# Performance work log

Measured on AMD Instinct MI355X. Metric: run time of the kernel, lower is better.

## Reference

```python
import jax, jax.numpy as jnp
import numpy as np

B, C, L = 8, 512, 2048


def setup_inputs() -> dict:
    key = jax.random.key(0)
    ks = jax.random.split(key, 7)
    s = 1.0 / np.sqrt(C)
    return {
        "x": jax.random.normal(ks[0], (B, C, L), dtype=jnp.float32),
        "Wq": jax.random.normal(ks[1], (C, C), dtype=jnp.float32) * s,
        "bq": jax.random.normal(ks[2], (C,), dtype=jnp.float32) * s,
        "Wk": jax.random.normal(ks[3], (C, C), dtype=jnp.float32) * s,
        "bk": jax.random.normal(ks[4], (C,), dtype=jnp.float32) * s,
        "Wv": jax.random.normal(ks[5], (C, C), dtype=jnp.float32) * s,
        "bv": jax.random.normal(ks[6], (C,), dtype=jnp.float32) * s,
    }


def reference(x, Wq, bq, Wk, bk, Wv, bv):
    # Conv1d(kernel_size=1) == per-position linear: [C_out, C_in] @ x[b,:,l]
    q = jnp.einsum('oi,bil->bol', Wq, x) + bq[None, :, None]  # [B, C, L]
    k = jnp.einsum('oi,bil->bol', Wk, x) + bk[None, :, None]
    v = jnp.einsum('oi,bil->bol', Wv, x) + bv[None, :, None]
    scale = 1.0 / jnp.sqrt(jnp.asarray(x.shape[1], dtype=x.dtype))
    # scores[b, l, m] = sum_c q[b,c,l] * k[b,c,m] / sqrt(C)
    scores = jnp.einsum('bcl,bcm->blm', q, k) * scale  # [B, L, L]
    attn = jax.nn.softmax(scores, axis=-1)
    # out[b, c, l] = sum_m v[b,c,m] * attn[b,l,m]   (== bmm(V, attn^T))
    return jnp.einsum('bcm,blm->bcl', v, attn)  # [B, C, L]
```

## Files before the change

### kernel.cpp

```cpp
#include <hip/hip_runtime.h>
#include <hip/hip_bf16.h>
#include <math.h>

#define B 8
#define C 512
#define L 2048

using bf16x8 = __bf16 __attribute__((ext_vector_type(8)));
using f32x4  = float __attribute__((ext_vector_type(4)));

#define MFMA(a, b, c) __builtin_amdgcn_mfma_f32_16x16x32_bf16((a), (b), (c), 0, 0, 0)
#define SC2 0.06375872f
#define SH2 -17.312340f

__device__ __forceinline__ unsigned short f2bf(float f) {
    unsigned int u; __builtin_memcpy(&u, &f, 4);
    u += 0x7FFF + ((u >> 16) & 1);
    return (unsigned short)(u >> 16);
}
__device__ __forceinline__ void load_lds16(const unsigned short* g, unsigned short* l) {
    __builtin_amdgcn_global_load_lds(
        (const __attribute__((address_space(1))) unsigned int*)g,
        (__attribute__((address_space(3))) unsigned int*)l, 16, 0, 0);
}

template<int MODE, int KDIM>
__device__ __forceinline__ void gemm_core(
    const unsigned short* __restrict__ A,
    const unsigned short* __restrict__ Bm,
    unsigned short* As, unsigned short* Bs,
    void* __restrict__ OutV, int ldo,
    float* __restrict__ ep)
{
    const int t = threadIdx.x;
    const int wave = t >> 6, lane = t & 63;
    const int ll = t & 15, quad = (t >> 4) & 3;
    const int lr = lane >> 2, chunk = lane & 3;
    const int wm = (wave & 1) * 64, wn = (wave >> 1) * 64;

    const unsigned short* gA0 = A  + (size_t)(wave * 32 + lr) * KDIM + chunk * 8;
    const unsigned short* gB0 = Bm + (size_t)(wave * 32 + lr) * KDIM + chunk * 8;
    unsigned short* lA0 = As + (wave * 32) * 32;
    unsigned short* lB0 = Bs + (wave * 32) * 32;
    const int P1 = 128 * 32;

    f32x4 acc[4][4];
#pragma unroll
    for (int i = 0; i < 4; ++i)
#pragma unroll
        for (int j = 0; j < 4; ++j) acc[i][j] = (f32x4){0.f, 0.f, 0.f, 0.f};

#pragma unroll 1
    for (int k0 = 0; k0 < KDIM; k0 += 64) {
        __syncthreads();
        load_lds16(gA0 + k0, lA0);
        load_lds16(gA0 + (size_t)16 * KDIM + k0, lA0 + 16 * 32);
        load_lds16(gA0 + k0 + 32, lA0 + P1);
        load_lds16(gA0 + (size_t)16 * KDIM + k0 + 32, lA0 + P1 + 16 * 32);
        load_lds16(gB0 + k0, lB0);
        load_lds16(gB0 + (size_t)16 * KDIM + k0, lB0 + 16 * 32);
        load_lds16(gB0 + k0 + 32, lB0 + P1);
        load_lds16(gB0 + (size_t)16 * KDIM + k0 + 32, lB0 + P1 + 16 * 32);
        __syncthreads();

#pragma unroll
        for (int p = 0; p < 2; ++p) {
            bf16x8 af[4], bf[4];
#pragma unroll
            for (int mi = 0; mi < 4; ++mi)
                af[mi] = *(const bf16x8*)&As[p * P1 + (wm + mi * 16 + ll) * 32 + quad * 8];
#pragma unroll
            for (int ni = 0; ni < 4; ++ni)
                bf[ni] = *(const bf16x8*)&Bs[p * P1 + (wn + ni * 16 + ll) * 32 + quad * 8];
#pragma unroll
            for (int mi = 0; mi < 4; ++mi)
#pragma unroll
                for (int ni = 0; ni < 4; ++ni)
                    acc[mi][ni] = MFMA(af[mi], bf[ni], acc[mi][ni]);
        }
    }

    float rpart[4][4];
    if (MODE == 2) {
#pragma unroll
        for (int mi = 0; mi < 4; ++mi)
#pragma unroll
            for (int r = 0; r < 4; ++r) rpart[mi][r] = 0.f;
    }

#pragma unroll
    for (int mi = 0; mi < 4; ++mi)
#pragma unroll
        for (int ni = 0; ni < 4; ++ni) {
            const int col = wn + ni * 16 + ll;
            float epc = 0.f;
            if (MODE == 0) epc = ep[col];
            if (MODE == 3) epc = 1.0f / ep[col];
#pragma unroll
            for (int r = 0; r < 4; ++r) {
                const int row = wm + mi * 16 + quad * 4 + r;
                float v = acc[mi][ni][r];
                if (MODE == 0)      v += epc;
                else if (MODE == 1) v += ep[row];
                else if (MODE == 2) { v = exp2f(fmaf(v, SC2, SH2)); rpart[mi][r] += v; }
                else                v *= epc;
                if (MODE == 3)
                    ((float*)OutV)[(size_t)row * ldo + col] = v;
                else
                    ((unsigned short*)OutV)[(size_t)row * ldo + col] = f2bf(v);
            }
        }

    if (MODE == 2) {
#pragma unroll
        for (int mi = 0; mi < 4; ++mi)
#pragma unroll
            for (int r = 0; r < 4; ++r) {
                float s = rpart[mi][r];
                s += __shfl_xor(s, 1, 64);
                s += __shfl_xor(s, 2, 64);
                s += __shfl_xor(s, 4, 64);
                s += __shfl_xor(s, 8, 64);
                if (ll == 0) atomicAdd(ep + wm + mi * 16 + quad * 4 + r, s);
            }
    }
}

__global__ __launch_bounds__(256) void xpose_cvt(
    const float* __restrict__ x, unsigned short* __restrict__ xt)
{
    __shared__ float tile[64][69];
    const int b = blockIdx.z, l0 = blockIdx.x * 64, c0 = blockIdx.y * 64;
    const int t = threadIdx.x;
    const int lx = t & 15, cy = t >> 4;
    const float* xb = x + (size_t)b * C * L;
#pragma unroll
    for (int p = 0; p < 4; ++p) {
        float4 v = *(const float4*)(xb + (size_t)(c0 + p * 16 + cy) * L + l0 + lx * 4);
        tile[p * 16 + cy][lx * 4 + 0] = v.x;
        tile[p * 16 + cy][lx * 4 + 1] = v.y;
        tile[p * 16 + cy][lx * 4 + 2] = v.z;
        tile[p * 16 + cy][lx * 4 + 3] = v.w;
    }
    __syncthreads();
    const int ocl = t & 15, ot = t >> 4;
    unsigned short* xtb = xt + (size_t)b * L * C;
#pragma unroll
    for (int p = 0; p < 4; ++p) {
        int ol = p * 16 + ot;
        union { unsigned short h[4]; uint2 u; } pk;
#pragma unroll
        for (int i = 0; i < 4; ++i) pk.h[i] = f2bf(tile[ocl * 4 + i][ol]);
        *(uint2*)(xtb + (size_t)(l0 + ol) * C + c0 + ocl * 4) = pk.u;
    }
}

__global__ __launch_bounds__(256) void wcvt(
    const float* __restrict__ Wq, const float* __restrict__ Wk,
    const float* __restrict__ Wv, unsigned short* __restrict__ o,
    float* __restrict__ rsum)
{
    if (blockIdx.x < 16) {
        float4 z = make_float4(0.f, 0.f, 0.f, 0.f);
        *(float4*)(rsum + (blockIdx.x * 256 + threadIdx.x) * 4) = z;
    }
    const int i = (blockIdx.x * 256 + threadIdx.x) * 4;
    const int which = i >> 18;
    const int off = i & 0x3FFFF;
    const float* src = (which == 0) ? Wq : (which == 1) ? Wk : Wv;
    float4 v = *(const float4*)(src + off);
    union { unsigned short h[4]; uint2 u; } pk;
    pk.h[0] = f2bf(v.x); pk.h[1] = f2bf(v.y); pk.h[2] = f2bf(v.z); pk.h[3] = f2bf(v.w);
    *(uint2*)(o + i) = pk.u;
}

__global__ __launch_bounds__(256) void qkv_gemm(
    const unsigned short* __restrict__ xt, const unsigned short* __restrict__ Wb,
    const float* __restrict__ bq, const float* __restrict__ bk,
    const float* __restrict__ bv,
    unsigned short* __restrict__ Qt, unsigned short* __restrict__ Kt,
    unsigned short* __restrict__ Vv)
{
    __shared__ unsigned short As[2 * 128 * 32], Bs[2 * 128 * 32];
    const int id = blockIdx.x;
    const int b = id & 7, r = id >> 3;
    const int which = r >> 6, tt = r & 63;
    const unsigned short* xtb = xt + (size_t)b * L * C;
    if (which < 2) {
        const int m0 = (tt & 15) * 128, n0 = (tt >> 4) * 128;
        const unsigned short* A  = xtb + (size_t)m0 * C;
        const unsigned short* Bm = Wb + (size_t)which * C * C + (size_t)n0 * C;
        unsigned short* Out = (which ? Kt : Qt) + (size_t)b * L * C
                              + (size_t)m0 * C + n0;
        gemm_core<0, C>(A, Bm, As, Bs, Out, C,
                        const_cast<float*>((which ? bk : bq) + n0));
    } else {
        const int m0 = (tt & 3) * 128, n0 = (tt >> 2) * 128;
        const unsigned short* A  = Wb + (size_t)2 * C * C + (size_t)m0 * C;
        const unsigned short* Bm = xtb + (size_t)n0 * C;
        unsigned short* Out = Vv + (size_t)b * C * L + (size_t)m0 * L + n0;
        gemm_core<1, C>(A, Bm, As, Bs, Out, L, const_cast<float*>(bv + m0));
    }
}

__global__ __launch_bounds__(256) void sc_exp(
    const unsigned short* __restrict__ Qt, const unsigned short* __restrict__ Kt,
    unsigned short* __restrict__ P, float* __restrict__ rsum,
    int hoff, int qrows, int mshift)
{
    __shared__ unsigned short As[2 * 128 * 32], Bs[2 * 128 * 32];
    const int id = blockIdx.x;
    const int b = id & 7, r = id >> 3;
    const int m0 = (r & ((1 << mshift) - 1)) * 128, n0 = (r >> mshift) * 128;
    const unsigned short* A  = Qt + (size_t)b * L * C + (size_t)(hoff + m0) * C;
    const unsigned short* Bm = Kt + (size_t)b * L * C + (size_t)n0 * C;
    unsigned short* Out = P + (size_t)b * qrows * L + (size_t)m0 * L + n0;
    float* ep = rsum + (size_t)b * L + hoff + m0;
    gemm_core<2, C>(A, Bm, As, Bs, Out, L, ep);
}

__global__ __launch_bounds__(256) void pv_gemm(
    const unsigned short* __restrict__ Vv, const unsigned short* __restrict__ P,
    const float* __restrict__ rsum, float* __restrict__ out,
    int hoff, int qrows)
{
    __shared__ unsigned short As[2 * 128 * 32], Bs[2 * 128 * 32];
    const int id = blockIdx.x;
    const int b = id & 7, r = id >> 3;
    const int m0 = (r & 3) * 128, n0 = (r >> 2) * 128;
    const unsigned short* A  = Vv + (size_t)b * C * L + (size_t)m0 * L;
    const unsigned short* Bm = P + (size_t)b * qrows * L + (size_t)n0 * L;
    float* Out = out + (size_t)b * C * L + (size_t)m0 * L + hoff + n0;
    float* ep = const_cast<float*>(rsum) + (size_t)b * L + hoff + n0;
    gemm_core<3, L>(A, Bm, As, Bs, Out, L, ep);
}

extern "C" void kernel_launch(void* const* d_in, const int* in_sizes, int n_in,
                              void* d_out, int out_size, void* d_ws, size_t ws_size,
                              hipStream_t stream) {
    const float* x  = (const float*)d_in[0];
    const float* Wq = (const float*)d_in[1];
    const float* bq = (const float*)d_in[2];
    const float* Wk = (const float*)d_in[3];
    const float* bk = (const float*)d_in[4];
    const float* Wv = (const float*)d_in[5];
    const float* bv = (const float*)d_in[6];
    float* out = (float*)d_out;

    const size_t BCL = (size_t)B * C * L;
    const bool fullP = ws_size >= 119078912ull;

    unsigned short* Qt = (unsigned short*)d_ws;
    unsigned short* Kt = Qt + BCL;
    unsigned short* Vv = Kt + BCL;
    unsigned short *Wb, *xt, *P;
    float* rsum;
    if (fullP) {
        Wb   = Vv + BCL;
        rsum = (float*)(Wb + (size_t)3 * C * C);
        xt   = (unsigned short*)(rsum + (size_t)B * L);
        P    = xt;
    } else {
        xt   = Vv + BCL;
        P    = xt;
        Wb   = P + (size_t)B * 1024 * L;
        rsum = (float*)(Wb + (size_t)3 * C * C);
    }

    xpose_cvt<<<dim3(L / 64, C / 64, B), 256, 0, stream>>>(x, xt);
    wcvt<<<dim3(3 * C * C / 1024), 256, 0, stream>>>(Wq, Wk, Wv, Wb, rsum);
    qkv_gemm<<<dim3(1536), 256, 0, stream>>>(xt, Wb, bq, bk, bv, Qt, Kt, Vv);

    if (fullP) {
        sc_exp<<<dim3(2048), 256, 0, stream>>>(Qt, Kt, P, rsum, 0, L, 4);
        pv_gemm<<<dim3(512), 256, 0, stream>>>(Vv, P, rsum, out, 0, L);
    } else {
        for (int h = 0; h < 2; ++h) {
            sc_exp<<<dim3(1024), 256, 0, stream>>>(Qt, Kt, P, rsum, h * 1024, 1024, 3);
            pv_gemm<<<dim3(256), 256, 0, stream>>>(Vv, P, rsum, out, h * 1024, 1024);
        }
    }
}
```

Measured before the change: 229.5 us.

## Replace scores GEMM with 256x256-tile 8-wave pipelined kernel using swizzled LDS

Adds a dedicated sc_exp2 kernel for the QK^T scores plus exp stage. It uses 256x256 output tiles with 512 threads, direct global-to-LDS loads into an XOR-swizzled double buffer, and loads interleaved with MFMA phases via barriers and s_setprio. The fused exp/row-sum epilogue moves out of the shared gemm_core into the new kernel. The aim is more data reuse per tile, fewer LDS bank conflicts and better load/compute overlap, at the cost of higher register pressure (8x4 accumulators) and fewer blocks in the grid.

```diff
diff --git a/kernel.cpp b/kernel.cpp
--- a/kernel.cpp
+++ b/kernel.cpp
@@ -12,6 +12,7 @@
 #define MFMA(a, b, c) __builtin_amdgcn_mfma_f32_16x16x32_bf16((a), (b), (c), 0, 0, 0)
 #define SC2 0.06375872f
 #define SH2 -17.312340f
+#define MEMFENCE() asm volatile("" ::: "memory")
 
 __device__ __forceinline__ unsigned short f2bf(float f) {
     unsigned int u; __builtin_memcpy(&u, &f, 4);
@@ -80,14 +81,6 @@
         }
     }
 
-    float rpart[4][4];
-    if (MODE == 2) {
-#pragma unroll
-        for (int mi = 0; mi < 4; ++mi)
-#pragma unroll
-            for (int r = 0; r < 4; ++r) rpart[mi][r] = 0.f;
-    }
-
 #pragma unroll
     for (int mi = 0; mi < 4; ++mi)
 #pragma unroll
@@ -102,7 +95,6 @@
                 float v = acc[mi][ni][r];
                 if (MODE == 0)      v += epc;
                 else if (MODE == 1) v += ep[row];
-                else if (MODE == 2) { v = exp2f(fmaf(v, SC2, SH2)); rpart[mi][r] += v; }
                 else                v *= epc;
                 if (MODE == 3)
                     ((float*)OutV)[(size_t)row * ldo + col] = v;
@@ -110,20 +102,6 @@
                     ((unsigned short*)OutV)[(size_t)row * ldo + col] = f2bf(v);
             }
         }
-
-    if (MODE == 2) {
-#pragma unroll
-        for (int mi = 0; mi < 4; ++mi)
-#pragma unroll
-            for (int r = 0; r < 4; ++r) {
-                float s = rpart[mi][r];
-                s += __shfl_xor(s, 1, 64);
-                s += __shfl_xor(s, 2, 64);
-                s += __shfl_xor(s, 4, 64);
-                s += __shfl_xor(s, 8, 64);
-                if (ll == 0) atomicAdd(ep + wm + mi * 16 + quad * 4 + r, s);
-            }
-    }
 }
 
 __global__ __launch_bounds__(256) void xpose_cvt(
@@ -203,20 +181,191 @@
     }
 }
 
-__global__ __launch_bounds__(256) void sc_exp(
+__global__ __launch_bounds__(512, 2) void sc_exp2(
     const unsigned short* __restrict__ Qt, const unsigned short* __restrict__ Kt,
     unsigned short* __restrict__ P, float* __restrict__ rsum,
     int hoff, int qrows, int mshift)
 {
-    __shared__ unsigned short As[2 * 128 * 32], Bs[2 * 128 * 32];
+    __shared__ unsigned short As[2][16384], Bs[2][16384];
+    constexpr int KD = C;
+    constexpr int NT = C / 64;
+
     const int id = blockIdx.x;
-    const int b = id & 7, r = id >> 3;
-    const int m0 = (r & ((1 << mshift) - 1)) * 128, n0 = (r >> mshift) * 128;
+    const int b = id & 7, rr = id >> 3;
+    const int m0 = (rr & ((1 << mshift) - 1)) * 256, n0 = (rr >> mshift) * 256;
     const unsigned short* A  = Qt + (size_t)b * L * C + (size_t)(hoff + m0) * C;
     const unsigned short* Bm = Kt + (size_t)b * L * C + (size_t)n0 * C;
     unsigned short* Out = P + (size_t)b * qrows * L + (size_t)m0 * L + n0;
     float* ep = rsum + (size_t)b * L + hoff + m0;
-    gemm_core<2, C>(A, Bm, As, Bs, Out, L, ep);
+
+    const int t = threadIdx.x;
+    const int wave = t >> 6, lane = t & 63;
+    const int ll = lane & 15, quad = lane >> 4;
+    const int wm = wave & 1, wn = wave >> 1;
+    const int r0 = t >> 3;
+    const int swz = ((t & 7) ^ (r0 & 7)) * 8;
+    const int sw8 = ll & 7;
+    const int c0 = (quad ^ sw8) * 8;
+    const int c1 = ((4 + quad) ^ sw8) * 8;
+    const int aB = wm * 8192 + ll * 64;
+    const int bB = wn * 4096 + ll * 64;
+
+    const unsigned short* gA = A  + (size_t)r0 * KD + swz;
+    const unsigned short* gB = Bm + (size_t)r0 * KD + swz;
+
+    f32x4 acc[8][4];
+#pragma unroll
+    for (int i = 0; i < 8; ++i)
+#pragma unroll
+        for (int j = 0; j < 4; ++j) acc[i][j] = (f32x4){0.f, 0.f, 0.f, 0.f};
+
+    {
+        unsigned short* sA0 = &As[0][0] + wave * 512;
+        unsigned short* sB0 = &Bs[0][0] + wave * 512;
+        unsigned short* sB1 = &Bs[1][0] + wave * 512;
+        load_lds16(gA,                          sA0);
+        load_lds16(gA + (size_t)64  * KD,       sA0 + 4096);
+        load_lds16(gA + (size_t)128 * KD,       sA0 + 8192);
+        load_lds16(gA + (size_t)192 * KD,       sA0 + 12288);
+        load_lds16(gB,                          sB0);
+        load_lds16(gB + (size_t)64  * KD,       sB0 + 4096);
+        load_lds16(gB + (size_t)128 * KD,       sB0 + 8192);
+        load_lds16(gB + (size_t)192 * KD,       sB0 + 12288);
+        load_lds16(gB + 64,                     sB1);
+        load_lds16(gB + (size_t)64  * KD + 64,  sB1 + 4096);
+        load_lds16(gB + (size_t)128 * KD + 64,  sB1 + 8192);
+        load_lds16(gB + (size_t)192 * KD + 64,  sB1 + 12288);
+        asm volatile("s_waitcnt vmcnt(4)" ::: "memory");
+        __builtin_amdgcn_sched_barrier(0);
+        MEMFENCE(); __builtin_amdgcn_s_barrier(); MEMFENCE();
+    }
+
+#pragma unroll 1
+    for (int kt = 0; kt < NT; ++kt) {
+        const int p = kt & 1;
+        const unsigned short* Ap = &As[p][0];
+        const unsigned short* Bp = &Bs[p][0];
+        const int kaOff = (kt + 1 < NT ? kt + 1 : 0) * 64;
+        const int kbOff = (kt + 2 < NT ? kt + 2 : 0) * 64;
+        unsigned short* stA = &As[(kt + 1) & 1][0] + wave * 512;
+        unsigned short* stB = &Bs[p][0] + wave * 512;
+
+        bf16x8 bfr[4][2], af[2][2];
+
+#pragma unroll
+        for (int ni = 0; ni < 4; ++ni) {
+            bfr[ni][0] = *(const bf16x8*)&Bp[bB + ni * 1024 + c0];
+            bfr[ni][1] = *(const bf16x8*)&Bp[bB + ni * 1024 + c1];
+        }
+#pragma unroll
+        for (int mi2 = 0; mi2 < 2; ++mi2) {
+            af[mi2][0] = *(const bf16x8*)&Ap[aB + mi2 * 1024 + c0];
+            af[mi2][1] = *(const bf16x8*)&Ap[aB + mi2 * 1024 + c1];
+        }
+        load_lds16(gA + kaOff,                    stA);
+        load_lds16(gA + (size_t)64 * KD + kaOff,  stA + 4096);
+        MEMFENCE(); __builtin_amdgcn_s_barrier(); MEMFENCE();
+        __builtin_amdgcn_s_setprio(1);
+#pragma unroll
+        for (int mi2 = 0; mi2 < 2; ++mi2)
+#pragma unroll
+            for (int ni = 0; ni < 4; ++ni) {
+                acc[mi2][ni] = MFMA(af[mi2][0], bfr[ni][0], acc[mi2][ni]);
+                acc[mi2][ni] = MFMA(af[mi2][1], bfr[ni][1], acc[mi2][ni]);
+            }
+        __builtin_amdgcn_s_setprio(0);
+        MEMFENCE(); __builtin_amdgcn_s_barrier(); MEMFENCE();
+
+#pragma unroll
+        for (int mi2 = 0; mi2 < 2; ++mi2) {
+            af[mi2][0] = *(const bf16x8*)&Ap[aB + 2048 + mi2 * 1024 + c0];
+            af[mi2][1] = *(const bf16x8*)&Ap[aB + 2048 + mi2 * 1024 + c1];
+        }
+        load_lds16(gA + (size_t)128 * KD + kaOff, stA + 8192);
+        load_lds16(gA + (size_t)192 * KD + kaOff, stA + 12288);
+        MEMFENCE(); __builtin_amdgcn_s_barrier(); MEMFENCE();
+        __builtin_amdgcn_s_setprio(1);
+#pragma unroll
+        for (int mi2 = 0; mi2 < 2; ++mi2)
+#pragma unroll
+            for (int ni = 0; ni < 4; ++ni) {
+                acc[2 + mi2][ni] = MFMA(af[mi2][0], bfr[ni][0], acc[2 + mi2][ni]);
+                acc[2 + mi2][ni] = MFMA(af[mi2][1], bfr[ni][1], acc[2 + mi2][ni]);
+            }
+        __builtin_amdgcn_s_setprio(0);
+        MEMFENCE(); __builtin_amdgcn_s_barrier(); MEMFENCE();
+
+#pragma unroll
+        for (int mi2 = 0; mi2 < 2; ++mi2) {
+            af[mi2][0] = *(const bf16x8*)&Ap[aB + 4096 + mi2 * 1024 + c0];
+            af[mi2][1] = *(const bf16x8*)&Ap[aB + 4096 + mi2 * 1024 + c1];
+        }
+        load_lds16(gB + kbOff,                    stB);
+        load_lds16(gB + (size_t)64 * KD + kbOff,  stB + 4096);
+        MEMFENCE(); __builtin_amdgcn_s_barrier(); MEMFENCE();
+        __builtin_amdgcn_s_setprio(1);
+#pragma unroll
+        for (int mi2 = 0; mi2 < 2; ++mi2)
+#pragma unroll
+            for (int ni = 0; ni < 4; ++ni) {
+                acc[4 + mi2][ni] = MFMA(af[mi2][0], bfr[ni][0], acc[4 + mi2][ni]);
+                acc[4 + mi2][ni] = MFMA(af[mi2][1], bfr[ni][1], acc[4 + mi2][ni]);
+            }
+        __builtin_amdgcn_s_setprio(0);
+        MEMFENCE(); __builtin_amdgcn_s_barrier(); MEMFENCE();
+
+#pragma unroll
+        for (int mi2 = 0; mi2 < 2; ++mi2) {
+            af[mi2][0] = *(const bf16x8*)&Ap[aB + 6144 + mi2 * 1024 + c0];
+            af[mi2][1] = *(const bf16x8*)&Ap[aB + 6144 + mi2 * 1024 + c1];
+        }
+        load_lds16(gB + (size_t)128 * KD + kbOff, stB + 8192);
+        load_lds16(gB + (size_t)192 * KD + kbOff, stB + 12288);
+        MEMFENCE(); __builtin_amdgcn_s_barrier(); MEMFENCE();
+        __builtin_amdgcn_s_setprio(1);
+#pragma unroll
+        for (int mi2 = 0; mi2 < 2; ++mi2)
+#pragma unroll
+            for (int ni = 0; ni < 4; ++ni) {
+                acc[6 + mi2][ni] = MFMA(af[mi2][0], bfr[ni][0], acc[6 + mi2][ni]);
+                acc[6 + mi2][ni] = MFMA(af[mi2][1], bfr[ni][1], acc[6 + mi2][ni]);
+            }
+        __builtin_amdgcn_s_setprio(0);
+        asm volatile("s_waitcnt vmcnt(4)" ::: "memory");
+        __builtin_amdgcn_sched_barrier(0);
+        MEMFENCE(); __builtin_amdgcn_s_barrier(); MEMFENCE();
+    }
+
+    float rpart[8][4];
+#pragma unroll
+    for (int mi = 0; mi < 8; ++mi)
+#pragma unroll
+        for (int r = 0; r < 4; ++r) rpart[mi][r] = 0.f;
+
+#pragma unroll
+    for (int mi = 0; mi < 8; ++mi)
+#pragma unroll
+        for (int ni = 0; ni < 4; ++ni) {
+            const int col = wn * 64 + ni * 16 + ll;
+#pragma unroll
+            for (int r = 0; r < 4; ++r) {
+                const int row = wm * 128 + mi * 16 + quad * 4 + r;
+                float v = exp2f(fmaf(acc[mi][ni][r], SC2, SH2));
+                rpart[mi][r] += v;
+                Out[(size_t)row * L + col] = f2bf(v);
+            }
+        }
+#pragma unroll
+    for (int mi = 0; mi < 8; ++mi)
+#pragma unroll
+        for (int r = 0; r < 4; ++r) {
+            float s = rpart[mi][r];
+            s += __shfl_xor(s, 1, 64);
+            s += __shfl_xor(s, 2, 64);
+            s += __shfl_xor(s, 4, 64);
+            s += __shfl_xor(s, 8, 64);
+            if (ll == 0) atomicAdd(ep + wm * 128 + mi * 16 + quad * 4 + r, s);
+        }
 }
 
 __global__ __launch_bounds__(256) void pv_gemm(
@@ -272,11 +421,11 @@
     qkv_gemm<<<dim3(1536), 256, 0, stream>>>(xt, Wb, bq, bk, bv, Qt, Kt, Vv);
 
     if (fullP) {
-        sc_exp<<<dim3(2048), 256, 0, stream>>>(Qt, Kt, P, rsum, 0, L, 4);
+        sc_exp2<<<dim3(512), 512, 0, stream>>>(Qt, Kt, P, rsum, 0, L, 3);
         pv_gemm<<<dim3(512), 256, 0, stream>>>(Vv, P, rsum, out, 0, L);
     } else {
         for (int h = 0; h < 2; ++h) {
-            sc_exp<<<dim3(1024), 256, 0, stream>>>(Qt, Kt, P, rsum, h * 1024, 1024, 3);
+            sc_exp2<<<dim3(256), 512, 0, stream>>>(Qt, Kt, P, rsum, h * 1024, 1024, 2);
             pv_gemm<<<dim3(256), 256, 0, stream>>>(Vv, P, rsum, out, h * 1024, 1024);
         }
     }
```

After: 232.4 us. Within noise of the previous version (+1.3%).

## Give score-exp GEMM its own 256x128 tile kernel with 512 threads and swizzled LDS

Applied to the files above, without the earlier changes.

Replaces the shared gemm_core path for the QK^T + exp step with a dedicated kernel. Each block now has 8 waves, computes a 256x128 output tile and steps K by 64, using an XOR-swizzled LDS layout to avoid bank conflicts. The goal is more data reuse per block, fewer barriers per K step, and fewer blocks to launch. The cost is a single LDS buffer with no double buffering, so loads and MFMA compute may overlap less. Register pressure under launch_bounds(512,6) is also a risk.

```diff
diff --git a/kernel.cpp b/kernel.cpp
--- a/kernel.cpp
+++ b/kernel.cpp
@@ -80,14 +80,6 @@
         }
     }
 
-    float rpart[4][4];
-    if (MODE == 2) {
-#pragma unroll
-        for (int mi = 0; mi < 4; ++mi)
-#pragma unroll
-            for (int r = 0; r < 4; ++r) rpart[mi][r] = 0.f;
-    }
-
 #pragma unroll
     for (int mi = 0; mi < 4; ++mi)
 #pragma unroll
@@ -102,7 +94,6 @@
                 float v = acc[mi][ni][r];
                 if (MODE == 0)      v += epc;
                 else if (MODE == 1) v += ep[row];
-                else if (MODE == 2) { v = exp2f(fmaf(v, SC2, SH2)); rpart[mi][r] += v; }
                 else                v *= epc;
                 if (MODE == 3)
                     ((float*)OutV)[(size_t)row * ldo + col] = v;
@@ -110,20 +101,6 @@
                     ((unsigned short*)OutV)[(size_t)row * ldo + col] = f2bf(v);
             }
         }
-
-    if (MODE == 2) {
-#pragma unroll
-        for (int mi = 0; mi < 4; ++mi)
-#pragma unroll
-            for (int r = 0; r < 4; ++r) {
-                float s = rpart[mi][r];
-                s += __shfl_xor(s, 1, 64);
-                s += __shfl_xor(s, 2, 64);
-                s += __shfl_xor(s, 4, 64);
-                s += __shfl_xor(s, 8, 64);
-                if (ll == 0) atomicAdd(ep + wm + mi * 16 + quad * 4 + r, s);
-            }
-    }
 }
 
 __global__ __launch_bounds__(256) void xpose_cvt(
@@ -203,20 +180,103 @@
     }
 }
 
-__global__ __launch_bounds__(256) void sc_exp(
+__global__ __launch_bounds__(512, 6) void sc_exp3(
     const unsigned short* __restrict__ Qt, const unsigned short* __restrict__ Kt,
     unsigned short* __restrict__ P, float* __restrict__ rsum,
     int hoff, int qrows, int mshift)
 {
-    __shared__ unsigned short As[2 * 128 * 32], Bs[2 * 128 * 32];
+    __shared__ unsigned short As[256 * 64];
+    __shared__ unsigned short Bs[128 * 64];
+    constexpr int KD = C;
+
     const int id = blockIdx.x;
-    const int b = id & 7, r = id >> 3;
-    const int m0 = (r & ((1 << mshift) - 1)) * 128, n0 = (r >> mshift) * 128;
+    const int b = id & 7, rr = id >> 3;
+    const int m0 = (rr & ((1 << mshift) - 1)) * 256, n0 = (rr >> mshift) * 128;
     const unsigned short* A  = Qt + (size_t)b * L * C + (size_t)(hoff + m0) * C;
     const unsigned short* Bm = Kt + (size_t)b * L * C + (size_t)n0 * C;
     unsigned short* Out = P + (size_t)b * qrows * L + (size_t)m0 * L + n0;
     float* ep = rsum + (size_t)b * L + hoff + m0;
-    gemm_core<2, C>(A, Bm, As, Bs, Out, L, ep);
+
+    const int t = threadIdx.x;
+    const int wave = t >> 6;
+    const int ll = t & 15, quad = (t >> 4) & 3;
+    const int wm = (wave & 3) * 64, wn = (wave >> 2) * 64;
+
+    const int r0 = t >> 3;
+    const int swz = ((t & 7) ^ (r0 & 7)) * 8;
+    const unsigned short* gA = A  + (size_t)r0 * KD + swz;
+    const unsigned short* gB = Bm + (size_t)r0 * KD + swz;
+    unsigned short* lA = As + wave * 512;
+    unsigned short* lB = Bs + wave * 512;
+
+    const int sw8 = ll & 7;
+
+    f32x4 acc[4][4];
+#pragma unroll
+    for (int i = 0; i < 4; ++i)
+#pragma unroll
+        for (int j = 0; j < 4; ++j) acc[i][j] = (f32x4){0.f, 0.f, 0.f, 0.f};
+
+#pragma unroll 1
+    for (int k0 = 0; k0 < KD; k0 += 64) {
+        __syncthreads();
+        load_lds16(gA + k0,                     lA);
+        load_lds16(gA + (size_t)64  * KD + k0,  lA + 64 * 64);
+        load_lds16(gA + (size_t)128 * KD + k0,  lA + 128 * 64);
+        load_lds16(gA + (size_t)192 * KD + k0,  lA + 192 * 64);
+        load_lds16(gB + k0,                     lB);
+        load_lds16(gB + (size_t)64  * KD + k0,  lB + 64 * 64);
+        __syncthreads();
+
+#pragma unroll
+        for (int p = 0; p < 2; ++p) {
+            bf16x8 af[4], bf[4];
+#pragma unroll
+            for (int mi = 0; mi < 4; ++mi)
+                af[mi] = *(const bf16x8*)&As[(wm + mi * 16 + ll) * 64
+                                             + ((p * 4 + quad) ^ sw8) * 8];
+#pragma unroll
+            for (int ni = 0; ni < 4; ++ni)
+                bf[ni] = *(const bf16x8*)&Bs[(wn + ni * 16 + ll) * 64
+                                             + ((p * 4 + quad) ^ sw8) * 8];
+#pragma unroll
+            for (int mi = 0; mi < 4; ++mi)
+#pragma unroll
+                for (int ni = 0; ni < 4; ++ni)
+                    acc[mi][ni] = MFMA(af[mi], bf[ni], acc[mi][ni]);
+        }
+    }
+
+    float rpart[4][4];
+#pragma unroll
+    for (int mi = 0; mi < 4; ++mi)
+#pragma unroll
+        for (int r = 0; r < 4; ++r) rpart[mi][r] = 0.f;
+
+#pragma unroll
+    for (int mi = 0; mi < 4; ++mi)
+#pragma unroll
+        for (int ni = 0; ni < 4; ++ni) {
+            const int col = wn + ni * 16 + ll;
+#pragma unroll
+            for (int r = 0; r < 4; ++r) {
+                const int row = wm + mi * 16 + quad * 4 + r;
+                float v = exp2f(fmaf(acc[mi][ni][r], SC2, SH2));
+                rpart[mi][r] += v;
+                Out[(size_t)row * L + col] = f2bf(v);
+            }
+        }
+#pragma unroll
+    for (int mi = 0; mi < 4; ++mi)
+#pragma unroll
+        for (int r = 0; r < 4; ++r) {
+            float s = rpart[mi][r];
+            s += __shfl_xor(s, 1, 64);
+            s += __shfl_xor(s, 2, 64);
+            s += __shfl_xor(s, 4, 64);
+            s += __shfl_xor(s, 8, 64);
+            if (ll == 0) atomicAdd(ep + wm + mi * 16 + quad * 4 + r, s);
+        }
 }
 
 __global__ __launch_bounds__(256) void pv_gemm(
@@ -272,11 +332,11 @@
     qkv_gemm<<<dim3(1536), 256, 0, stream>>>(xt, Wb, bq, bk, bv, Qt, Kt, Vv);
 
     if (fullP) {
-        sc_exp<<<dim3(2048), 256, 0, stream>>>(Qt, Kt, P, rsum, 0, L, 4);
+        sc_exp3<<<dim3(1024), 512, 0, stream>>>(Qt, Kt, P, rsum, 0, L, 3);
         pv_gemm<<<dim3(512), 256, 0, stream>>>(Vv, P, rsum, out, 0, L);
     } else {
         for (int h = 0; h < 2; ++h) {
-            sc_exp<<<dim3(1024), 256, 0, stream>>>(Qt, Kt, P, rsum, h * 1024, 1024, 3);
+            sc_exp3<<<dim3(512), 512, 0, stream>>>(Qt, Kt, P, rsum, h * 1024, 1024, 2);
             pv_gemm<<<dim3(256), 256, 0, stream>>>(Vv, P, rsum, out, h * 1024, 1024);
         }
     }
```

Result: slower. 350.2 us (+52.6%).
